# Performance work log

Measured on AMD Instinct MI355X. Metric: run time of the kernel, lower is better.

The kernel has to match this reference:

```python
import jax, jax.numpy as jnp
import numpy as np

T_KD = 20.0      # KL_divergence temperature
T_THR = 6.0      # Threshold_weights temperature
EPS = 1e-05


def _margin(o, gathered):
    # torch.sort descending, take top-2; margin only when target is the argmax value
    top2 = jax.lax.top_k(o, 2)[0]                      # [B, 2]
    return jnp.where(top2[:, 0] == gathered, top2[:, 0] - top2[:, 1], 0.0)


def _forward(outputs1, outputs2, outputs3, outputs4, out_s, targets):
    B = targets.shape[0]
    idx = jnp.arange(B)
    mimic = (outputs1 + outputs2 + outputs3 + outputs4) / 4.0

    teachers = [outputs1, outputs2, outputs3, outputs4, mimic]
    gathered = [t[idx, targets] for t in teachers]      # each [B]

    # C = min over gathered target logits of the 4 real teachers
    C = jnp.minimum(jnp.minimum(gathered[0].min(), gathered[1].min()),
                    jnp.minimum(gathered[2].min(), gathered[3].min()))
    # if C < 0: shift everything by (-C + eps); else no shift
    shift = jnp.where(C < 0, -C + EPS, 0.0)

    shifted = [t + shift for t in teachers]
    g_shift = [g + shift for g in gathered]

    # Threshold_weights: margin per branch, softmax over 5 branches
    preds = jnp.stack([_margin(s, g) for s, g in zip(shifted, g_shift)], axis=1)  # [B,5]
    out_threshold = jax.nn.softmax(preds / T_THR, axis=1)

    # max over the 4 (shifted) teacher logit tensors
    max_preds = jnp.maximum(jnp.maximum(shifted[0].max(), shifted[1].max()),
                            jnp.maximum(shifted[2].max(), shifted[3].max()))

    # per-sample CE of student (shared across branches)
    log_p_s = jax.nn.log_softmax(out_s, axis=1)
    CE = -log_p_s[idx, targets]                          # [B]

    log_ps_T = jax.nn.log_softmax(out_s / T_KD, axis=1)  # [B,C]

    def branch_loss(teacher, g_s):
        w2 = g_s / max_preds          # weights2
        w1 = 1.0 - w2                 # weights1
        log_pt = jax.nn.log_softmax(teacher / T_KD, axis=1)
        p_t = jnp.exp(log_pt)
        KD = jnp.sum(p_t * (log_pt - log_ps_T), axis=1) * (T_KD * T_KD)  # [B]
        return w1 * CE + w2 * KD

    # KD/CE use the ORIGINAL (unshifted) teacher logits
    losses = jnp.stack([branch_loss(t, g) for t, g in zip(teachers, g_shift)], axis=1)  # [B,5]
    return jnp.mean(jnp.sum(out_threshold * losses, axis=1))


def setup_inputs() -> dict:
    key = jax.random.key(0)
    ks = jax.random.split(key, 6)
    B, C = 8192, 1000
    return {
        "outputs1": jax.random.normal(ks[0], (B, C), dtype=jnp.float32),
        "outputs2": jax.random.normal(ks[1], (B, C), dtype=jnp.float32),
        "outputs3": jax.random.normal(ks[2], (B, C), dtype=jnp.float32),
        "outputs4": jax.random.normal(ks[3], (B, C), dtype=jnp.float32),
        "out_s": jax.random.normal(ks[4], (B, C), dtype=jnp.float32),
        "targets": jax.random.randint(ks[5], (B,), 0, C, dtype=jnp.int64 if jax.config.jax_enable_x64 else jnp.int32),
    }


def reference(outputs1, outputs2, outputs3, outputs4, out_s, targets):
    return _forward(outputs1, outputs2, outputs3, outputs4, out_s, targets)
```

## Files before the change

### kernel.cpp

```cpp
#include <hip/hip_runtime.h>
#include <math.h>

#define NB 8192
#define NC 1000
#define NF4 250


#define LOG2E 1.4426950408889634f
#define LN2   0.6931471805599453f

__device__ __forceinline__ float fexp2(float x) { return __builtin_amdgcn_exp2f(x); }
__device__ __forceinline__ float flog2(float x) { return __builtin_amdgcn_logf(x); }

template <int CTRL>
__device__ __forceinline__ float dpp_mov(float v, float ident) {
  return __uint_as_float((unsigned)__builtin_amdgcn_update_dpp(
      (int)__float_as_uint(ident), (int)__float_as_uint(v), CTRL, 0xF, 0xF,
      false));
}

__device__ __forceinline__ float dppredsum(float v) {
  v += dpp_mov<0x111>(v, 0.f);
  v += dpp_mov<0x112>(v, 0.f);
  v += dpp_mov<0x114>(v, 0.f);
  v += dpp_mov<0x118>(v, 0.f);
  v += dpp_mov<0x142>(v, 0.f);
  v += dpp_mov<0x143>(v, 0.f);
  return v;
}

__device__ __forceinline__ void dppredtop2(float& t1, float& t2) {
  const float NI = -INFINITY;
#define T2STEP(C)                                   \
  {                                                 \
    float i1 = dpp_mov<C>(t1, NI);                  \
    float i2 = dpp_mov<C>(t2, NI);                  \
    t2 = fmaxf(fmaxf(t2, i2), fminf(t1, i1));       \
    t1 = fmaxf(t1, i1);                             \
  }
  T2STEP(0x111) T2STEP(0x112) T2STEP(0x114) T2STEP(0x118)
  T2STEP(0x142) T2STEP(0x143)
#undef T2STEP
}

__device__ __forceinline__ float wredsum(float v) {
#pragma unroll
  for (int m = 32; m >= 1; m >>= 1) v += __shfl_xor(v, m, 64);
  return v;
}
__device__ __forceinline__ float wredmax(float v) {
#pragma unroll
  for (int m = 32; m >= 1; m >>= 1) v = fmaxf(v, __shfl_xor(v, m, 64));
  return v;
}
__device__ __forceinline__ float wredmin(float v) {
#pragma unroll
  for (int m = 32; m >= 1; m >>= 1) v = fminf(v, __shfl_xor(v, m, 64));
  return v;
}
__device__ __forceinline__ float f4get(const float4& v, int e) {
  return e == 0 ? v.x : e == 1 ? v.y : e == 2 ? v.z : v.w;
}

__device__ __forceinline__ void proc_chunk(
    const float4& c1, const float4& c2, const float4& c3, const float4& c4,
    const float4& cs, float t1[5], float t2[5], float Z[5], float S1[5],
    float& Z1, float& Z20) {
  const float K20 = LOG2E / 20.0f;
#pragma unroll
  for (int e = 0; e < 4; ++e) {
    float w0 = f4get(c1, e);
    float w1 = f4get(c2, e);
    float w2 = f4get(c3, e);
    float w3 = f4get(c4, e);
    float wsv = f4get(cs, e);
    float wm = ((w0 + w1) + w2 + w3) * 0.25f;
    float w[5] = {w0, w1, w2, w3, wm};
#pragma unroll
    for (int t = 0; t < 5; ++t) {
      t2[t] = fmaxf(t2[t], fminf(t1[t], w[t]));
      t1[t] = fmaxf(t1[t], w[t]);
      float et = fexp2(w[t] * K20);
      Z[t] += et;
      S1[t] = fmaf(et, w[t] - wsv, S1[t]);
    }
    Z1 += fexp2(wsv * LOG2E);
    Z20 += fexp2(wsv * K20);
  }
}

__global__ __launch_bounds__(256, 4) void k_rowstats(
    const float* __restrict__ o1, const float* __restrict__ o2,
    const float* __restrict__ o3, const float* __restrict__ o4,
    const float* __restrict__ os, const int* __restrict__ tg,
    float* __restrict__ ws, float* __restrict__ out) {
  const int lane = threadIdx.x & 63;
  const int wv = threadIdx.x >> 6;
  const int row = (blockIdx.x << 2) + wv;
  const size_t base = (size_t)row * NC;

  if (blockIdx.x == 0 && threadIdx.x == 0) out[0] = 0.0f;

  const int target = tg[row];
  const float g1 = o1[base + target];
  const float g2 = o2[base + target];
  const float g3 = o3[base + target];
  const float g4 = o4[base + target];
  const float gs = os[base + target];

  float4 A1[4], A2[4], A3[4], A4[4], AS[4];
#pragma unroll
  for (int i = 0; i < 4; ++i) {
    int f = lane + (i << 6);
    if (f > NF4 - 1) f = NF4 - 1;
    A1[i] = ((const float4*)(o1 + base))[f];
    A2[i] = ((const float4*)(o2 + base))[f];
    A3[i] = ((const float4*)(o3 + base))[f];
    A4[i] = ((const float4*)(o4 + base))[f];
    AS[i] = ((const float4*)(os + base))[f];
  }

  float t1[5], t2[5], Z[5], S1[5];
#pragma unroll
  for (int t = 0; t < 5; ++t) {
    t1[t] = -INFINITY; t2[t] = -INFINITY; Z[t] = 0.f; S1[t] = 0.f;
  }
  float Z1 = 0.f, Z20 = 0.f;

  proc_chunk(A1[0], A2[0], A3[0], A4[0], AS[0], t1, t2, Z, S1, Z1, Z20);
  proc_chunk(A1[1], A2[1], A3[1], A4[1], AS[1], t1, t2, Z, S1, Z1, Z20);
  proc_chunk(A1[2], A2[2], A3[2], A4[2], AS[2], t1, t2, Z, S1, Z1, Z20);
  if (lane < 58)
    proc_chunk(A1[3], A2[3], A3[3], A4[3], AS[3], t1, t2, Z, S1, Z1, Z20);

#pragma unroll
  for (int t = 0; t < 5; ++t) dppredtop2(t1[t], t2[t]);
#pragma unroll
  for (int t = 0; t < 5; ++t) { Z[t] = dppredsum(Z[t]); S1[t] = dppredsum(S1[t]); }
  Z1 = dppredsum(Z1);
  Z20 = dppredsum(Z20);

  if (lane == 63) {
    const float gm = ((g1 + g2) + g3 + g4) * 0.25f;
    float gg[5] = {g1, g2, g3, g4, gm};

    const float lse_s = flog2(Z20) * LN2;
    const float CE = flog2(Z1) * LN2 - gs;

#pragma unroll
    for (int t = 0; t < 5; ++t) {
      float lse_t = flog2(Z[t]) * LN2;
      float KD = 400.0f * (S1[t] / (20.0f * Z[t]) - lse_t + lse_s);
      float margin = (t1[t] == gg[t]) ? (t1[t] - t2[t]) : 0.0f;
      ws[(size_t)t * NB + row] = margin;
      ws[(size_t)(5 + t) * NB + row] = gg[t];
      ws[(size_t)(10 + t) * NB + row] = KD;
    }
    ws[(size_t)15 * NB + row] = CE;
    ws[(size_t)16 * NB + row] = fminf(fminf(g1, g2), fminf(g3, g4));
    ws[(size_t)17 * NB + row] = fmaxf(fmaxf(t1[0], t1[1]), fmaxf(t1[2], t1[3]));
  }
}

__global__ __launch_bounds__(256) void k_final(const float* __restrict__ ws,
                                               float* __restrict__ out) {
  const int tid = threadIdx.x;
  const int lane = tid & 63, wv = tid >> 6;
  __shared__ float sMn[4], sMx[4], sA[4];

  float mn = INFINITY, mx = -INFINITY;
  const float4* mnp = (const float4*)(ws + (size_t)16 * NB);
  const float4* mxp = (const float4*)(ws + (size_t)17 * NB);
#pragma unroll 1
  for (int r4 = tid; r4 < NB / 4; r4 += 256) {
    float4 a = mnp[r4];
    float4 b = mxp[r4];
    mn = fminf(mn, fminf(fminf(a.x, a.y), fminf(a.z, a.w)));
    mx = fmaxf(mx, fmaxf(fmaxf(b.x, b.y), fmaxf(b.z, b.w)));
  }
  mn = wredmin(mn);
  mx = wredmax(mx);
  if (lane == 0) { sMn[wv] = mn; sMx[wv] = mx; }
  __syncthreads();
  const float a = fminf(fminf(sMn[0], sMn[1]), fminf(sMn[2], sMn[3]));
  const float b = fmaxf(fmaxf(sMx[0], sMx[1]), fmaxf(sMx[2], sMx[3]));
  const float shift = (a < 0.0f) ? (-a + 1e-5f) : 0.0f;
  const float maxp = b + shift;

  const int r = blockIdx.x * 256 + tid;
  const float K6 = LOG2E / 6.0f;

  float m[5], e[5];
#pragma unroll
  for (int t = 0; t < 5; ++t) m[t] = ws[(size_t)t * NB + r];
  float pm = fmaxf(fmaxf(fmaxf(m[0], m[1]), fmaxf(m[2], m[3])), m[4]);
  float Zl = 0.0f;
#pragma unroll
  for (int t = 0; t < 5; ++t) { e[t] = fexp2((m[t] - pm) * K6); Zl += e[t]; }
  float ce = ws[(size_t)15 * NB + r];
  float rl = 0.0f;
#pragma unroll
  for (int t = 0; t < 5; ++t) {
    float g = ws[(size_t)(5 + t) * NB + r];
    float kd = ws[(size_t)(10 + t) * NB + r];
    float w2 = (g + shift) / maxp;
    float loss = (1.0f - w2) * ce + w2 * kd;
    rl += e[t] * loss;
  }
  float acc = rl / Zl;

  acc = wredsum(acc);
  if (lane == 0) sA[wv] = acc;
  __syncthreads();
  if (tid == 0) {
    float tot = (sA[0] + sA[1]) + (sA[2] + sA[3]);
    atomicAdd(out, tot * (1.0f / 8192.0f));
  }
}

extern "C" void kernel_launch(void* const* d_in, const int* in_sizes, int n_in,
                              void* d_out, int out_size, void* d_ws, size_t ws_size,
                              hipStream_t stream) {
  const float* o1 = (const float*)d_in[0];
  const float* o2 = (const float*)d_in[1];
  const float* o3 = (const float*)d_in[2];
  const float* o4 = (const float*)d_in[3];
  const float* os = (const float*)d_in[4];
  const int* tg = (const int*)d_in[5];
  float* ws = (float*)d_ws;
  float* out = (float*)d_out;

  k_rowstats<<<NB / 4, 256, 0, stream>>>(o1, o2, o3, o4, os, tg, ws, out);
  k_final<<<NB / 256, 256, 0, stream>>>(ws, out);
}
```

Measured before the change: 185.6 us.

## Stage row chunks through LDS with async global_load_lds double buffering

Global loads of the five input rows in the row-stats kernel now go straight into LDS through global_load_lds, into a two-slot buffer per wave, with manual vmcnt/lgkmcnt waits. This replaces loading all four chunks into registers up front. The aim is lower register pressure and overlap of the next chunk's fetch with the math on the current one. The final kernel's reduction loop is also fully unrolled. The risks are the cost of the extra LDS round trip and correctness that depends on the hand-written wait counts.

```diff
diff --git a/kernel.cpp b/kernel.cpp
--- a/kernel.cpp
+++ b/kernel.cpp
@@ -11,6 +11,19 @@
 
 __device__ __forceinline__ float fexp2(float x) { return __builtin_amdgcn_exp2f(x); }
 __device__ __forceinline__ float flog2(float x) { return __builtin_amdgcn_logf(x); }
+
+#define VMWAIT(N)                                        \
+  asm volatile("s_waitcnt vmcnt(" #N ")" ::: "memory");  \
+  __builtin_amdgcn_sched_barrier(0)
+#define LGKM0                                            \
+  asm volatile("s_waitcnt lgkmcnt(0)" ::: "memory");     \
+  __builtin_amdgcn_sched_barrier(0)
+
+typedef const __attribute__((address_space(1))) unsigned int gu32;
+typedef __attribute__((address_space(3))) unsigned int lu32;
+__device__ __forceinline__ void stage16(const void* g, void* l) {
+  __builtin_amdgcn_global_load_lds((gu32*)g, (lu32*)l, 16, 0, 0);
+}
 
 template <int CTRL>
 __device__ __forceinline__ float dpp_mov(float v, float ident) {
@@ -99,7 +112,23 @@
   const int row = (blockIdx.x << 2) + wv;
   const size_t base = (size_t)row * NC;
 
+  __shared__ float4 lds[4][2][5][64];
+
   if (blockIdx.x == 0 && threadIdx.x == 0) out[0] = 0.0f;
+
+#define STAGE(i, b)                                                       \
+  do {                                                                    \
+    int f_ = lane + ((i) << 6);                                           \
+    if (f_ > NF4 - 1) f_ = NF4 - 1;    \
+    stage16((const float4*)(o1 + base) + f_, &lds[wv][b][0][0]);          \
+    stage16((const float4*)(o2 + base) + f_, &lds[wv][b][1][0]);          \
+    stage16((const float4*)(o3 + base) + f_, &lds[wv][b][2][0]);          \
+    stage16((const float4*)(o4 + base) + f_, &lds[wv][b][3][0]);          \
+    stage16((const float4*)(os + base) + f_, &lds[wv][b][4][0]);          \
+  } while (0)
+
+  STAGE(0, 0);
+  STAGE(1, 1);
 
   const int target = tg[row];
   const float g1 = o1[base + target];
@@ -108,30 +137,41 @@
   const float g4 = o4[base + target];
   const float gs = os[base + target];
 
-  float4 A1[4], A2[4], A3[4], A4[4], AS[4];
-#pragma unroll
-  for (int i = 0; i < 4; ++i) {
-    int f = lane + (i << 6);
-    if (f > NF4 - 1) f = NF4 - 1;
-    A1[i] = ((const float4*)(o1 + base))[f];
-    A2[i] = ((const float4*)(o2 + base))[f];
-    A3[i] = ((const float4*)(o3 + base))[f];
-    A4[i] = ((const float4*)(o4 + base))[f];
-    AS[i] = ((const float4*)(os + base))[f];
-  }
-
   float t1[5], t2[5], Z[5], S1[5];
 #pragma unroll
   for (int t = 0; t < 5; ++t) {
     t1[t] = -INFINITY; t2[t] = -INFINITY; Z[t] = 0.f; S1[t] = 0.f;
   }
   float Z1 = 0.f, Z20 = 0.f;
-
-  proc_chunk(A1[0], A2[0], A3[0], A4[0], AS[0], t1, t2, Z, S1, Z1, Z20);
-  proc_chunk(A1[1], A2[1], A3[1], A4[1], AS[1], t1, t2, Z, S1, Z1, Z20);
-  proc_chunk(A1[2], A2[2], A3[2], A4[2], AS[2], t1, t2, Z, S1, Z1, Z20);
+  float4 r1, r2, r3, r4, rs;
+
+#define READC(b)                                                          \
+  r1 = lds[wv][b][0][lane]; r2 = lds[wv][b][1][lane];                     \
+  r3 = lds[wv][b][2][lane]; r4 = lds[wv][b][3][lane];                     \
+  rs = lds[wv][b][4][lane];
+
+  VMWAIT(5);
+  READC(0);
+  LGKM0;
+  STAGE(2, 0);
+  proc_chunk(r1, r2, r3, r4, rs, t1, t2, Z, S1, Z1, Z20);
+
+  VMWAIT(5);
+  READC(1);
+  LGKM0;
+  STAGE(3, 1);
+  proc_chunk(r1, r2, r3, r4, rs, t1, t2, Z, S1, Z1, Z20);
+
+  VMWAIT(5);
+  READC(0);
+  LGKM0;
+  proc_chunk(r1, r2, r3, r4, rs, t1, t2, Z, S1, Z1, Z20);
+
+  VMWAIT(0);
+  READC(1);
+  LGKM0;
   if (lane < 58)
-    proc_chunk(A1[3], A2[3], A3[3], A4[3], AS[3], t1, t2, Z, S1, Z1, Z20);
+    proc_chunk(r1, r2, r3, r4, rs, t1, t2, Z, S1, Z1, Z20);
 
 #pragma unroll
   for (int t = 0; t < 5; ++t) dppredtop2(t1[t], t2[t]);
@@ -160,6 +200,8 @@
     ws[(size_t)16 * NB + row] = fminf(fminf(g1, g2), fminf(g3, g4));
     ws[(size_t)17 * NB + row] = fmaxf(fmaxf(t1[0], t1[1]), fmaxf(t1[2], t1[3]));
   }
+#undef STAGE
+#undef READC
 }
 
 __global__ __launch_bounds__(256) void k_final(const float* __restrict__ ws,
@@ -171,8 +213,9 @@
   float mn = INFINITY, mx = -INFINITY;
   const float4* mnp = (const float4*)(ws + (size_t)16 * NB);
   const float4* mxp = (const float4*)(ws + (size_t)17 * NB);
-#pragma unroll 1
-  for (int r4 = tid; r4 < NB / 4; r4 += 256) {
+#pragma unroll
+  for (int k = 0; k < 8; ++k) {
+    int r4 = tid + (k << 8);
     float4 a = mnp[r4];
     float4 b = mxp[r4];
     mn = fminf(mn, fminf(fminf(a.x, a.y), fminf(a.z, a.w)));
```

Measured after the change: 185.2 us. No clear change (-0.2%).
